# Kernel optimization log

Hardware: AMD Instinct MI355X
Metric: run time of the kernel (lower is better)

The kernel has to match this reference:

```python
import jax, jax.numpy as jnp
import numpy as np

N0, N1, N2, N3 = 400000, 100000, 20000, 4096
IN_F, HID_F, OUT_F = 256, 256, 128
E0, E1, E2 = 1500000, 200000, 40960


def setup_inputs() -> dict:
    key = jax.random.key(0)
    ks = jax.random.split(key, 16)
    inp = {}
    inp['feat'] = jax.random.normal(ks[0], (N0, IN_F), dtype=jnp.float32)
    inp['e0_src'] = jax.random.randint(ks[1], (E0,), 0, N0)
    inp['e0_dst'] = jax.random.randint(ks[2], (E0,), 0, N1)
    inp['e1_src'] = jax.random.randint(ks[3], (E1,), 0, N1)
    inp['e1_dst'] = jax.random.randint(ks[4], (E1,), 0, N2)
    inp['e2_src'] = jax.random.randint(ks[5], (E2,), 0, N2)
    inp['e2_dst'] = jax.random.randint(ks[6], (E2,), 0, N3)
    # SAGEConv params: fc_self and fc_neigh weights (in,out) + shared bias
    def lin(k, fi, fo):
        s = 1.0 / np.sqrt(fi)
        return jax.random.uniform(k, (fi, fo), jnp.float32, -s, s)
    inp['w_self0'] = lin(ks[7], IN_F, HID_F)
    inp['w_neigh0'] = lin(ks[8], IN_F, HID_F)
    inp['b0'] = jnp.zeros((HID_F,), jnp.float32)
    inp['w_self1'] = lin(ks[9], HID_F, HID_F)
    inp['w_neigh1'] = lin(ks[10], HID_F, HID_F)
    inp['b1'] = jnp.zeros((HID_F,), jnp.float32)
    inp['w_self2'] = lin(ks[11], HID_F, OUT_F)
    inp['w_neigh2'] = lin(ks[12], HID_F, OUT_F)
    inp['b2'] = jnp.zeros((OUT_F,), jnp.float32)
    return inp


def _sage_conv(h, src, dst, n_dst, w_self, w_neigh, b, act):
    # mean aggregation of src-node features onto dst nodes (irregular gather + segment reduce)
    msgs = h[src]                                                  # [E, F]
    s = jax.ops.segment_sum(msgs, dst, num_segments=n_dst)        # [n_dst, F]
    cnt = jax.ops.segment_sum(jnp.ones((src.shape[0], 1), h.dtype), dst, num_segments=n_dst)
    h_neigh = s / jnp.maximum(cnt, 1.0)
    out = h[:n_dst] @ w_self + h_neigh @ w_neigh + b
    return jax.nn.relu(out) if act else out


def reference(feat, e0_src, e0_dst, e1_src, e1_dst, e2_src, e2_dst,
              w_self0, w_neigh0, b0, w_self1, w_neigh1, b1, w_self2, w_neigh2, b2):
    # dropout is identity (eval mode)
    h = _sage_conv(feat, e0_src, e0_dst, N1, w_self0, w_neigh0, b0, act=True)
    h = _sage_conv(h, e1_src, e1_dst, N2, w_self1, w_neigh1, b1, act=True)
    h = _sage_conv(h, e2_src, e2_dst, N3, w_self2, w_neigh2, b2, act=False)
    return h
```

## Files before the change

kernel.cpp:

```cpp
#include <hip/hip_runtime.h>
#include <hip/hip_bf16.h>


static constexpr int kN1 = 100000, kN2 = 20000, kN3 = 4096;
static constexpr int kE0 = 1500000, kE1 = 200000, kE2 = 40960;

using bf8v  = __attribute__((ext_vector_type(8))) short;
using f32x4 = __attribute__((ext_vector_type(4))) float;

__device__ __forceinline__ unsigned short f2bu(float f) {
    __hip_bfloat16 h = __float2bfloat16(f);
    return *reinterpret_cast<unsigned short*>(&h);
}
__device__ __forceinline__ float bu2f_lo(unsigned u) {
    unsigned b = u << 16; return *reinterpret_cast<float*>(&b);
}
__device__ __forceinline__ float bu2f_hi(unsigned u) {
    unsigned b = u & 0xffff0000u; return *reinterpret_cast<float*>(&b);
}

static constexpr int CB  = 50000;
static constexpr int C0B = (kE0 + 255) / 256;
static constexpr int C1B = (kE1 + 255) / 256;
static constexpr int C2B = (kE2 + 255) / 256;
static constexpr int PW0B = 512, PW1B = 512, PW2B = 256;
static constexpr int M4_0 = kN1 / 4, M4_1 = kN2 / 4, M4_2 = kN3 / 4;
static constexpr int B0 = (M4_0 + 255) / 256;
static constexpr int B1 = (M4_1 + 255) / 256;
static constexpr int B2 = (M4_2 + 255) / 256;
static constexpr int BSCAN = B0 + B1 + B2;
static constexpr int ZN4 = 496384 / 16;
static constexpr int ZB  = (ZN4 + 255) / 256;
static constexpr int ET = kE0 + kE1 + kE2;
static constexpr int FB = (ET / 8 + 255) / 256;

__global__ __launch_bounds__(256) void k_zero(int4* __restrict__ p)
{
    int i = blockIdx.x * 256 + threadIdx.x;
    if (i < ZN4) p[i] = make_int4(0, 0, 0, 0);
}

template <bool BIG>
__global__ __launch_bounds__(256) void k_phase0(
    const float4* __restrict__ feat4, uint4* __restrict__ featbf,
    const int* __restrict__ e0d, const int* __restrict__ e1d,
    const int* __restrict__ e2d,
    int* __restrict__ cnt0, int* __restrict__ cnt1, int* __restrict__ cnt2,
    const float* __restrict__ ws0, const float* __restrict__ wn0,
    const float* __restrict__ ws1, const float* __restrict__ wn1,
    const float* __restrict__ ws2, const float* __restrict__ wn2,
    unsigned short* __restrict__ wt0, unsigned short* __restrict__ wt1,
    unsigned short* __restrict__ wt2)
{
    int b = blockIdx.x;
    const int tid = threadIdx.x;
    if (BIG) {
        if (b < CB) {
            int i = b * 256 + tid;
            float4 a = feat4[2 * i], c = feat4[2 * i + 1];
            uint4 o;
            o.x = (unsigned)f2bu(a.x) | ((unsigned)f2bu(a.y) << 16);
            o.y = (unsigned)f2bu(a.z) | ((unsigned)f2bu(a.w) << 16);
            o.z = (unsigned)f2bu(c.x) | ((unsigned)f2bu(c.y) << 16);
            o.w = (unsigned)f2bu(c.z) | ((unsigned)f2bu(c.w) << 16);
            featbf[i] = o;
            return;
        }
        b -= CB;
    }
    if (b < C0B) {
        int e = b * 256 + tid;
        if (e < kE0) atomicAdd(cnt0 + e0d[e], 1);
        return;
    }
    b -= C0B;
    if (b < C1B) {
        int e = b * 256 + tid;
        if (e < kE1) atomicAdd(cnt1 + e1d[e], 1);
        return;
    }
    b -= C1B;
    if (b < C2B) {
        int e = b * 256 + tid;
        if (e < kE2) atomicAdd(cnt2 + e2d[e], 1);
        return;
    }
    b -= C2B;
    if (b < PW0B) {
        int idx = b * 256 + tid;
        int n = idx >> 9, k = idx & 511;
        wt0[idx] = f2bu(k < 256 ? ws0[k * 256 + n] : wn0[(k - 256) * 256 + n]);
        return;
    }
    b -= PW0B;
    if (b < PW1B) {
        int idx = b * 256 + tid;
        int n = idx >> 9, k = idx & 511;
        wt1[idx] = f2bu(k < 256 ? ws1[k * 256 + n] : wn1[(k - 256) * 256 + n]);
        return;
    }
    b -= PW1B;
    {
        int idx = b * 256 + tid;
        int n = idx >> 9, k = idx & 511;
        wt2[idx] = f2bu(k < 256 ? ws2[k * 128 + n] : wn2[(k - 256) * 128 + n]);
    }
}

__global__ __launch_bounds__(256) void k_bsum_all(
    const int* __restrict__ cnt0, const int* __restrict__ cnt1,
    const int* __restrict__ cnt2, int* __restrict__ bsum)
{
    const int* cnt; int lb, M4, bo;
    int b = blockIdx.x;
    if (b < B0)            { cnt = cnt0; lb = b;            M4 = M4_0; bo = 0; }
    else if (b < B0 + B1)  { cnt = cnt1; lb = b - B0;       M4 = M4_1; bo = B0; }
    else                   { cnt = cnt2; lb = b - B0 - B1;  M4 = M4_2; bo = B0 + B1; }
    __shared__ int wsum[4];
    int idx = lb * 256 + threadIdx.x;
    int ts = 0;
    if (idx < M4) {
        int4 v = reinterpret_cast<const int4*>(cnt)[idx];
        ts = v.x + v.y + v.z + v.w;
    }
#pragma unroll
    for (int off = 32; off > 0; off >>= 1) ts += __shfl_down(ts, off, 64);
    if ((threadIdx.x & 63) == 0) wsum[threadIdx.x >> 6] = ts;
    __syncthreads();
    if (threadIdx.x == 0)
        bsum[bo + lb] = wsum[0] + wsum[1] + wsum[2] + wsum[3];
}

__global__ __launch_bounds__(256) void k_bapply_all(
    const int* __restrict__ cnt0, const int* __restrict__ cnt1,
    const int* __restrict__ cnt2, const int* __restrict__ bsum,
    int* __restrict__ rp0, int* __restrict__ rp1, int* __restrict__ rp2)
{
    const int* cnt; int* rp; int lb, M4, lo;
    int b = blockIdx.x;
    if (b < B0)            { cnt = cnt0; rp = rp0; lb = b;           M4 = M4_0; lo = 0; }
    else if (b < B0 + B1)  { cnt = cnt1; rp = rp1; lb = b - B0;      M4 = M4_1; lo = B0; }
    else                   { cnt = cnt2; rp = rp2; lb = b - B0 - B1; M4 = M4_2; lo = B0 + B1; }
    __shared__ int sscan[BSCAN];
    __shared__ int wsum[4];
    __shared__ int wexcl[4];
    __shared__ int blockbase;
    const int tid = threadIdx.x;
    const int lane = tid & 63;
    const int wid = tid >> 6;
    if (tid < BSCAN) sscan[tid] = bsum[tid];
    __syncthreads();
    if (tid == 0) {
        int s = 0;
        for (int i = lo; i < lo + lb; ++i) s += sscan[i];
        blockbase = s;
    }
    int idx = lb * 256 + tid;
    int4 v = make_int4(0, 0, 0, 0);
    if (idx < M4) v = reinterpret_cast<const int4*>(cnt)[idx];
    int ts = v.x + v.y + v.z + v.w;
    int incl = ts;
#pragma unroll
    for (int off = 1; off < 64; off <<= 1) {
        int t = __shfl_up(incl, off, 64);
        if (lane >= off) incl += t;
    }
    if (lane == 63) wsum[wid] = incl;
    __syncthreads();
    if (tid < 4) {
        int e = 0;
        for (int i = 0; i < tid; ++i) e += wsum[i];
        wexcl[tid] = e;
    }
    __syncthreads();
    if (idx < M4) {
        int base = blockbase + wexcl[wid] + (incl - ts);
        int4 o;
        o.x = base;
        o.y = base + v.x;
        o.z = base + v.x + v.y;
        o.w = base + v.x + v.y + v.z;
        reinterpret_cast<int4*>(rp)[idx] = o;
    }
}

__global__ __launch_bounds__(256) void k_fill_all(
    const int* __restrict__ e0s, const int* __restrict__ e0d,
    const int* __restrict__ e1s, const int* __restrict__ e1d,
    const int* __restrict__ e2s, const int* __restrict__ e2d,
    int* __restrict__ rp0, int* __restrict__ rp1, int* __restrict__ rp2,
    int* __restrict__ csr0, int* __restrict__ csr1, int* __restrict__ csr2)
{
    const int t = blockIdx.x * 256 + threadIdx.x;
    const int T = FB * 256;
    int ss[8], dd[8], pos[8];
    int* rpp[8];
    int* cp[8];
    bool ok[8];
#pragma unroll
    for (int i = 0; i < 8; ++i) {
        int e = t + i * T;
        ok[i] = e < ET;
        ss[i] = 0; dd[i] = 0; rpp[i] = rp0; cp[i] = csr0;
        if (ok[i]) {
            if (e < kE0) {
                ss[i] = e0s[e]; dd[i] = e0d[e];
            } else if (e < kE0 + kE1) {
                int le = e - kE0;
                ss[i] = e1s[le]; dd[i] = e1d[le]; rpp[i] = rp1; cp[i] = csr1;
            } else {
                int le = e - kE0 - kE1;
                ss[i] = e2s[le]; dd[i] = e2d[le]; rpp[i] = rp2; cp[i] = csr2;
            }
        }
    }
#pragma unroll
    for (int i = 0; i < 8; ++i)
        if (ok[i]) pos[i] = atomicAdd(rpp[i] + dd[i], 1);
#pragma unroll
    for (int i = 0; i < 8; ++i)
        if (ok[i]) cp[i][pos[i]] = ss[i];
}

__global__ __launch_bounds__(256) void k_gather_agg_b(
    const unsigned short* __restrict__ h, const int* __restrict__ csr,
    const int* __restrict__ rp_end, const int* __restrict__ cnt,
    unsigned short* __restrict__ agg, int M)
{
    int d = blockIdx.x * 4 + (threadIdx.x >> 6);
    if (d >= M) return;
    const int lane = threadIdx.x & 63;
    const int half = lane >> 5;
    const int l32 = lane & 31;
    int c = cnt[d], end = rp_end[d], start = end - c;
    float a[8] = {0.f, 0.f, 0.f, 0.f, 0.f, 0.f, 0.f, 0.f};
    for (int chunk = start; chunk < end; chunk += 64) {
        int n = end - chunk; if (n > 64) n = 64;
        int mysrc = (lane < n) ? csr[chunk + lane] : 0;
#pragma unroll 4
        for (int e = 0; e < n; e += 2) {
            int ie = e + half;
            int s = __shfl(mysrc, ie, 64);
            if (ie < n) {
                uint4 v = *reinterpret_cast<const uint4*>(
                    h + (size_t)s * 256 + l32 * 8);
                a[0] += bu2f_lo(v.x); a[1] += bu2f_hi(v.x);
                a[2] += bu2f_lo(v.y); a[3] += bu2f_hi(v.y);
                a[4] += bu2f_lo(v.z); a[5] += bu2f_hi(v.z);
                a[6] += bu2f_lo(v.w); a[7] += bu2f_hi(v.w);
            }
        }
    }
#pragma unroll
    for (int j = 0; j < 8; ++j) a[j] += __shfl(a[j], lane ^ 32, 64);
    if (half == 0) {
        float inv = 1.0f / (float)(c > 1 ? c : 1);
        uint4 o;
        o.x = (unsigned)f2bu(a[0] * inv) | ((unsigned)f2bu(a[1] * inv) << 16);
        o.y = (unsigned)f2bu(a[2] * inv) | ((unsigned)f2bu(a[3] * inv) << 16);
        o.z = (unsigned)f2bu(a[4] * inv) | ((unsigned)f2bu(a[5] * inv) << 16);
        o.w = (unsigned)f2bu(a[6] * inv) | ((unsigned)f2bu(a[7] * inv) << 16);
        *reinterpret_cast<uint4*>(agg + (size_t)d * 256 + l32 * 8) = o;
    }
}

__global__ __launch_bounds__(256) void k_gather_agg_f(
    const float* __restrict__ h, const int* __restrict__ csr,
    const int* __restrict__ rp_end, const int* __restrict__ cnt,
    unsigned short* __restrict__ agg, int M)
{
    int d = blockIdx.x * 4 + (threadIdx.x >> 6);
    if (d >= M) return;
    int lane = threadIdx.x & 63;
    int c = cnt[d], end = rp_end[d], start = end - c;
    float a0 = 0.f, a1 = 0.f, a2 = 0.f, a3 = 0.f;
    for (int chunk = start; chunk < end; chunk += 64) {
        int n = end - chunk; if (n > 64) n = 64;
        int mysrc = (lane < n) ? csr[chunk + lane] : 0;
#pragma unroll 4
        for (int e = 0; e < n; ++e) {
            int s = __shfl(mysrc, e, 64);
            float4 v = reinterpret_cast<const float4*>(h + (size_t)s * 256)[lane];
            a0 += v.x; a1 += v.y; a2 += v.z; a3 += v.w;
        }
    }
    float inv = 1.0f / (float)(c > 1 ? c : 1);
    ushort4 o;
    o.x = f2bu(a0 * inv); o.y = f2bu(a1 * inv);
    o.z = f2bu(a2 * inv); o.w = f2bu(a3 * inv);
    *reinterpret_cast<ushort4*>(agg + (size_t)d * 256 + lane * 4) = o;
}

template <int ACT, bool A0F32, bool OUTF32>
__global__ __launch_bounds__(256) void k_mfma_gemm(
    const void* __restrict__ A0v, const unsigned short* __restrict__ A1,
    const unsigned short* __restrict__ WT, const float* __restrict__ bias,
    void* __restrict__ outv, int M, int N)
{
    __shared__ unsigned short sA[128 * 72];
    __shared__ unsigned short sB[128 * 72];
    const int tid = threadIdx.x;
    const int lane = tid & 63;
    const int w = tid >> 6;
    const int wr = w >> 1, wc = w & 1;
    const int row0 = blockIdx.x * 128;
    const int col0 = blockIdx.y * 128;

    f32x4 acc[4][4] = {};

    for (int p = 0; p < 8; ++p) {
        const int kc0 = p * 64;
        if (kc0 < 256) {
            if constexpr (A0F32) {
                const float* src = (const float*)A0v;
#pragma unroll
                for (int ps = 0; ps < 8; ++ps) {
                    int flat = (ps * 256 + tid) * 4;
                    int r = flat >> 6, cc = flat & 63;
                    int row = row0 + r; row = row < M ? row : M - 1;
                    float4 v = *reinterpret_cast<const float4*>(
                        src + (size_t)row * 256 + kc0 + cc);
                    ushort4 b4;
                    b4.x = f2bu(v.x); b4.y = f2bu(v.y);
                    b4.z = f2bu(v.z); b4.w = f2bu(v.w);
                    *reinterpret_cast<ushort4*>(&sA[r * 72 + cc]) = b4;
                }
            } else {
                const unsigned short* src = (const unsigned short*)A0v;
#pragma unroll
                for (int ps = 0; ps < 4; ++ps) {
                    int f8 = ps * 256 + tid;
                    int r = f8 >> 3, c8 = f8 & 7;
                    int row = row0 + r; row = row < M ? row : M - 1;
                    uint4 v = *reinterpret_cast<const uint4*>(
                        src + (size_t)row * 256 + kc0 + c8 * 8);
                    *reinterpret_cast<uint4*>(&sA[r * 72 + c8 * 8]) = v;
                }
            }
        } else {
#pragma unroll
            for (int ps = 0; ps < 4; ++ps) {
                int f8 = ps * 256 + tid;
                int r = f8 >> 3, c8 = f8 & 7;
                int row = row0 + r; row = row < M ? row : M - 1;
                uint4 v = *reinterpret_cast<const uint4*>(
                    A1 + (size_t)row * 256 + (kc0 - 256) + c8 * 8);
                *reinterpret_cast<uint4*>(&sA[r * 72 + c8 * 8]) = v;
            }
        }
#pragma unroll
        for (int ps = 0; ps < 4; ++ps) {
            int f8 = ps * 256 + tid;
            int r = f8 >> 3, c8 = f8 & 7;
            uint4 v = *reinterpret_cast<const uint4*>(
                WT + (size_t)(col0 + r) * 512 + kc0 + c8 * 8);
            *reinterpret_cast<uint4*>(&sB[r * 72 + c8 * 8]) = v;
        }
        __syncthreads();
#pragma unroll
        for (int ks = 0; ks < 64; ks += 32) {
            const int lr = lane & 15;
            const int kk = ks + (lane >> 4) * 8;
            bf8v af[4], bfr[4];
#pragma unroll
            for (int m = 0; m < 4; ++m)
                af[m] = *reinterpret_cast<const bf8v*>(
                    &sA[(wr * 64 + m * 16 + lr) * 72 + kk]);
#pragma unroll
            for (int n = 0; n < 4; ++n)
                bfr[n] = *reinterpret_cast<const bf8v*>(
                    &sB[(wc * 64 + n * 16 + lr) * 72 + kk]);
#pragma unroll
            for (int m = 0; m < 4; ++m)
#pragma unroll
                for (int n = 0; n < 4; ++n)
                    acc[m][n] = __builtin_amdgcn_mfma_f32_16x16x32_bf16(
                        af[m], bfr[n], acc[m][n], 0, 0, 0);
        }
        __syncthreads();
    }

    const int lc = lane & 15;
    const int lr4 = (lane >> 4) * 4;
#pragma unroll
    for (int n = 0; n < 4; ++n) {
        int col = col0 + wc * 64 + n * 16 + lc;
        float bb = bias[col];
#pragma unroll
        for (int m = 0; m < 4; ++m) {
#pragma unroll
            for (int j = 0; j < 4; ++j) {
                int row = row0 + wr * 64 + m * 16 + lr4 + j;
                if (row < M) {
                    float v = acc[m][n][j] + bb;
                    if (ACT) v = fmaxf(v, 0.f);
                    if constexpr (OUTF32)
                        ((float*)outv)[(size_t)row * N + col] = v;
                    else
                        ((unsigned short*)outv)[(size_t)row * N + col] = f2bu(v);
                }
            }
        }
    }
}

extern "C" void kernel_launch(void* const* d_in, const int* in_sizes, int n_in,
                              void* d_out, int out_size, void* d_ws, size_t ws_size,
                              hipStream_t stream) {
    const float* feat = (const float*)d_in[0];
    const int* e0s = (const int*)d_in[1];
    const int* e0d = (const int*)d_in[2];
    const int* e1s = (const int*)d_in[3];
    const int* e1d = (const int*)d_in[4];
    const int* e2s = (const int*)d_in[5];
    const int* e2d = (const int*)d_in[6];
    const float* ws0 = (const float*)d_in[7];
    const float* wn0 = (const float*)d_in[8];
    const float* b0 = (const float*)d_in[9];
    const float* ws1 = (const float*)d_in[10];
    const float* wn1 = (const float*)d_in[11];
    const float* b1 = (const float*)d_in[12];
    const float* ws2 = (const float*)d_in[13];
    const float* wn2 = (const float*)d_in[14];
    const float* b2 = (const float*)d_in[15];
    float* out = (float*)d_out;

    char* base = (char*)d_ws;
    const bool big = ws_size >= 330000000ull;
    unsigned short* featbf = nullptr;
    size_t off = 0;
    if (big) { featbf = (unsigned short*)base; off += 204800000ull; }
    unsigned short* aggb = (unsigned short*)(base + off); off += 51200000ull;
    unsigned short* h1b  = (unsigned short*)(base + off); off += 51200000ull;
    unsigned short* h2b  = (unsigned short*)(base + off); off += 10240000ull;
    unsigned short* wt0  = (unsigned short*)(base + off); off += 262144ull;
    unsigned short* wt1  = (unsigned short*)(base + off); off += 262144ull;
    unsigned short* wt2  = (unsigned short*)(base + off); off += 131072ull;
    int* csr0 = (int*)(base + off); off += 6000000ull;
    int* csr1 = (int*)(base + off); off += 800000ull;
    int* csr2 = (int*)(base + off); off += 163840ull;
    int* cnt0 = (int*)(base + off); off += 400000ull;
    int* cnt1 = (int*)(base + off); off += 80000ull;
    int* cnt2 = (int*)(base + off); off += 16384ull;
    int* rp0  = (int*)(base + off); off += 400000ull;
    int* rp1  = (int*)(base + off); off += 80000ull;
    int* rp2  = (int*)(base + off); off += 16384ull;
    int* bsum = (int*)(base + off); off += 512ull;

    k_zero<<<ZB, 256, 0, stream>>>((int4*)cnt0);

    if (big)
        k_phase0<true><<<CB + C0B + C1B + C2B + PW0B + PW1B + PW2B, 256, 0, stream>>>(
            (const float4*)feat, (uint4*)featbf, e0d, e1d, e2d,
            cnt0, cnt1, cnt2, ws0, wn0, ws1, wn1, ws2, wn2, wt0, wt1, wt2);
    else
        k_phase0<false><<<C0B + C1B + C2B + PW0B + PW1B + PW2B, 256, 0, stream>>>(
            nullptr, nullptr, e0d, e1d, e2d,
            cnt0, cnt1, cnt2, ws0, wn0, ws1, wn1, ws2, wn2, wt0, wt1, wt2);

    k_bsum_all<<<BSCAN, 256, 0, stream>>>(cnt0, cnt1, cnt2, bsum);
    k_bapply_all<<<BSCAN, 256, 0, stream>>>(
        cnt0, cnt1, cnt2, bsum, rp0, rp1, rp2);
    k_fill_all<<<FB, 256, 0, stream>>>(
        e0s, e0d, e1s, e1d, e2s, e2d,
        rp0, rp1, rp2, csr0, csr1, csr2);

    if (big) {
        k_gather_agg_b<<<(kN1 + 3) / 4, 256, 0, stream>>>(
            featbf, csr0, rp0, cnt0, aggb, kN1);
        k_mfma_gemm<1, false, false><<<dim3(782, 2), 256, 0, stream>>>(
            featbf, aggb, wt0, b0, h1b, kN1, 256);
    } else {
        k_gather_agg_f<<<(kN1 + 3) / 4, 256, 0, stream>>>(
            feat, csr0, rp0, cnt0, aggb, kN1);
        k_mfma_gemm<1, true, false><<<dim3(782, 2), 256, 0, stream>>>(
            feat, aggb, wt0, b0, h1b, kN1, 256);
    }

    k_gather_agg_b<<<(kN2 + 3) / 4, 256, 0, stream>>>(
        h1b, csr1, rp1, cnt1, aggb, kN2);
    k_mfma_gemm<1, false, false><<<dim3(157, 2), 256, 0, stream>>>(
        h1b, aggb, wt1, b1, h2b, kN2, 256);

    k_gather_agg_b<<<(kN3 + 3) / 4, 256, 0, stream>>>(
        h2b, csr2, rp2, cnt2, aggb, kN3);
    k_mfma_gemm<0, false, true><<<dim3(32, 1), 256, 0, stream>>>(
        h2b, aggb, wt2, b2, out, kN3, 128);
}
```

Measured before the change: 528.8 us.

## Record per-edge rank during counting to drop atomics from CSR fill

The counting pass now stores each edge's return value from atomicAdd (its rank within its destination segment). The CSR fill kernel computes each slot as the row start plus that rank, using plain reads instead of a second round of atomics on the row pointers. Gather kernels now read row pointers as starts instead of ends. This removes 1.74M contended atomics and makes the CSR order deterministic within a pass. The cost is writing and then reading about 7MB of rank arrays, plus a larger workspace threshold for the big path.

```diff
diff --git a/kernel.cpp b/kernel.cpp
--- a/kernel.cpp
+++ b/kernel.cpp
@@ -46,6 +46,7 @@
     const int* __restrict__ e0d, const int* __restrict__ e1d,
     const int* __restrict__ e2d,
     int* __restrict__ cnt0, int* __restrict__ cnt1, int* __restrict__ cnt2,
+    int* __restrict__ er0, int* __restrict__ er1, int* __restrict__ er2,
     const float* __restrict__ ws0, const float* __restrict__ wn0,
     const float* __restrict__ ws1, const float* __restrict__ wn1,
     const float* __restrict__ ws2, const float* __restrict__ wn2,
@@ -70,19 +71,19 @@
     }
     if (b < C0B) {
         int e = b * 256 + tid;
-        if (e < kE0) atomicAdd(cnt0 + e0d[e], 1);
+        if (e < kE0) er0[e] = atomicAdd(cnt0 + e0d[e], 1);
         return;
     }
     b -= C0B;
     if (b < C1B) {
         int e = b * 256 + tid;
-        if (e < kE1) atomicAdd(cnt1 + e1d[e], 1);
+        if (e < kE1) er1[e] = atomicAdd(cnt1 + e1d[e], 1);
         return;
     }
     b -= C1B;
     if (b < C2B) {
         int e = b * 256 + tid;
-        if (e < kE2) atomicAdd(cnt2 + e2d[e], 1);
+        if (e < kE2) er2[e] = atomicAdd(cnt2 + e2d[e], 1);
         return;
     }
     b -= C2B;
@@ -188,43 +189,48 @@
     const int* __restrict__ e0s, const int* __restrict__ e0d,
     const int* __restrict__ e1s, const int* __restrict__ e1d,
     const int* __restrict__ e2s, const int* __restrict__ e2d,
-    int* __restrict__ rp0, int* __restrict__ rp1, int* __restrict__ rp2,
+    const int* __restrict__ er0, const int* __restrict__ er1,
+    const int* __restrict__ er2,
+    const int* __restrict__ rp0, const int* __restrict__ rp1,
+    const int* __restrict__ rp2,
     int* __restrict__ csr0, int* __restrict__ csr1, int* __restrict__ csr2)
 {
     const int t = blockIdx.x * 256 + threadIdx.x;
     const int T = FB * 256;
-    int ss[8], dd[8], pos[8];
-    int* rpp[8];
+    int ss[8], dd[8], rr[8], pos[8];
+    const int* rpp[8];
     int* cp[8];
     bool ok[8];
 #pragma unroll
     for (int i = 0; i < 8; ++i) {
         int e = t + i * T;
         ok[i] = e < ET;
-        ss[i] = 0; dd[i] = 0; rpp[i] = rp0; cp[i] = csr0;
+        ss[i] = 0; dd[i] = 0; rr[i] = 0; rpp[i] = rp0; cp[i] = csr0;
         if (ok[i]) {
             if (e < kE0) {
-                ss[i] = e0s[e]; dd[i] = e0d[e];
+                ss[i] = e0s[e]; dd[i] = e0d[e]; rr[i] = er0[e];
             } else if (e < kE0 + kE1) {
                 int le = e - kE0;
-                ss[i] = e1s[le]; dd[i] = e1d[le]; rpp[i] = rp1; cp[i] = csr1;
+                ss[i] = e1s[le]; dd[i] = e1d[le]; rr[i] = er1[le];
+                rpp[i] = rp1; cp[i] = csr1;
             } else {
                 int le = e - kE0 - kE1;
-                ss[i] = e2s[le]; dd[i] = e2d[le]; rpp[i] = rp2; cp[i] = csr2;
+                ss[i] = e2s[le]; dd[i] = e2d[le]; rr[i] = er2[le];
+                rpp[i] = rp2; cp[i] = csr2;
             }
         }
     }
 #pragma unroll
     for (int i = 0; i < 8; ++i)
-        if (ok[i]) pos[i] = atomicAdd(rpp[i] + dd[i], 1);
+        if (ok[i]) pos[i] = rpp[i][dd[i]];
 #pragma unroll
     for (int i = 0; i < 8; ++i)
-        if (ok[i]) cp[i][pos[i]] = ss[i];
+        if (ok[i]) cp[i][pos[i] + rr[i]] = ss[i];
 }
 
 __global__ __launch_bounds__(256) void k_gather_agg_b(
     const unsigned short* __restrict__ h, const int* __restrict__ csr,
-    const int* __restrict__ rp_end, const int* __restrict__ cnt,
+    const int* __restrict__ rp_start, const int* __restrict__ cnt,
     unsigned short* __restrict__ agg, int M)
 {
     int d = blockIdx.x * 4 + (threadIdx.x >> 6);
@@ -232,7 +238,7 @@
     const int lane = threadIdx.x & 63;
     const int half = lane >> 5;
     const int l32 = lane & 31;
-    int c = cnt[d], end = rp_end[d], start = end - c;
+    int c = cnt[d], start = rp_start[d], end = start + c;
     float a[8] = {0.f, 0.f, 0.f, 0.f, 0.f, 0.f, 0.f, 0.f};
     for (int chunk = start; chunk < end; chunk += 64) {
         int n = end - chunk; if (n > 64) n = 64;
@@ -266,13 +272,13 @@
 
 __global__ __launch_bounds__(256) void k_gather_agg_f(
     const float* __restrict__ h, const int* __restrict__ csr,
-    const int* __restrict__ rp_end, const int* __restrict__ cnt,
+    const int* __restrict__ rp_start, const int* __restrict__ cnt,
     unsigned short* __restrict__ agg, int M)
 {
     int d = blockIdx.x * 4 + (threadIdx.x >> 6);
     if (d >= M) return;
     int lane = threadIdx.x & 63;
-    int c = cnt[d], end = rp_end[d], start = end - c;
+    int c = cnt[d], start = rp_start[d], end = start + c;
     float a0 = 0.f, a1 = 0.f, a2 = 0.f, a3 = 0.f;
     for (int chunk = start; chunk < end; chunk += 64) {
         int n = end - chunk; if (n > 64) n = 64;
@@ -426,7 +432,7 @@
     float* out = (float*)d_out;
 
     char* base = (char*)d_ws;
-    const bool big = ws_size >= 330000000ull;
+    const bool big = ws_size >= 345000000ull;
     unsigned short* featbf = nullptr;
     size_t off = 0;
     if (big) { featbf = (unsigned short*)base; off += 204800000ull; }
@@ -446,24 +452,29 @@
     int* rp1  = (int*)(base + off); off += 80000ull;
     int* rp2  = (int*)(base + off); off += 16384ull;
     int* bsum = (int*)(base + off); off += 512ull;
+    int* er0  = (int*)(base + off); off += 6000000ull;
+    int* er1  = (int*)(base + off); off += 800000ull;
+    int* er2  = (int*)(base + off); off += 163840ull;
 
     k_zero<<<ZB, 256, 0, stream>>>((int4*)cnt0);
 
     if (big)
         k_phase0<true><<<CB + C0B + C1B + C2B + PW0B + PW1B + PW2B, 256, 0, stream>>>(
             (const float4*)feat, (uint4*)featbf, e0d, e1d, e2d,
-            cnt0, cnt1, cnt2, ws0, wn0, ws1, wn1, ws2, wn2, wt0, wt1, wt2);
+            cnt0, cnt1, cnt2, er0, er1, er2,
+            ws0, wn0, ws1, wn1, ws2, wn2, wt0, wt1, wt2);
     else
         k_phase0<false><<<C0B + C1B + C2B + PW0B + PW1B + PW2B, 256, 0, stream>>>(
             nullptr, nullptr, e0d, e1d, e2d,
-            cnt0, cnt1, cnt2, ws0, wn0, ws1, wn1, ws2, wn2, wt0, wt1, wt2);
+            cnt0, cnt1, cnt2, er0, er1, er2,
+            ws0, wn0, ws1, wn1, ws2, wn2, wt0, wt1, wt2);
 
     k_bsum_all<<<BSCAN, 256, 0, stream>>>(cnt0, cnt1, cnt2, bsum);
     k_bapply_all<<<BSCAN, 256, 0, stream>>>(
         cnt0, cnt1, cnt2, bsum, rp0, rp1, rp2);
     k_fill_all<<<FB, 256, 0, stream>>>(
         e0s, e0d, e1s, e1d, e2s, e2d,
-        rp0, rp1, rp2, csr0, csr1, csr2);
+        er0, er1, er2, rp0, rp1, rp2, csr0, csr1, csr2);
 
     if (big) {
         k_gather_agg_b<<<(kN1 + 3) / 4, 256, 0, stream>>>(
```

Result: faster. 472.5 us, median of 2 (-10.6%).
